# Optimization experiments

Hardware: AMD Instinct MI355X
Metric: run time of the kernel (lower is better)

Reference implementation:

```python
import jax, jax.numpy as jnp
import numpy as np

B, N, M, DK, DV, H = 4, 2048, 2048, 1024, 1024, 16
DKP = ((DK + H - 1) // H) * H  # 1024
DVP = ((DV + H - 1) // H) * H  # 1024


def setup_inputs() -> dict:
    key = jax.random.key(0)
    ks = jax.random.split(key, 12)
    s = 0.02
    return {
        "queries": jax.random.normal(ks[0], (B, N, DK), jnp.float32),
        "keys": jax.random.normal(ks[1], (B, M, DK), jnp.float32),
        "values": jax.random.normal(ks[2], (B, M, DV), jnp.float32),
        "presence": jnp.ones((B, M), jnp.float32),
        "n_heads": H,
        "wq": jax.random.normal(ks[3], (DK, DKP), jnp.float32) * s,
        "bq": jnp.zeros((DKP,), jnp.float32),
        "wk": jax.random.normal(ks[4], (DK, DKP), jnp.float32) * s,
        "bk": jnp.zeros((DKP,), jnp.float32),
        "wv": jax.random.normal(ks[5], (DV, DVP), jnp.float32) * s,
        "bv": jnp.zeros((DVP,), jnp.float32),
        "wo": jax.random.normal(ks[6], (DVP, DV), jnp.float32) * s,
        "bo": jnp.zeros((DV,), jnp.float32),
    }


def reference(queries, keys, values, presence, n_heads, wq, bq, wk, bk, wv, bv, wo, bo):
    b, n, _ = queries.shape
    m = keys.shape[1]
    h = n_heads
    # projections
    q = (queries @ wq + bq).reshape(b, n, h, -1)  # [B,N,H,dh]
    k = (keys @ wk + bk).reshape(b, m, h, -1)     # [B,M,H,dh]
    v = (values @ wv + bv).reshape(b, m, h, -1)   # [B,M,H,dv]
    dh = q.shape[-1]
    # scores: per-head scale is sqrt(per-head key dim), as in qkv_attention
    logits = jnp.einsum("bnhd,bmhd->bhnm", q, k)
    logits = logits - (1.0 - presence)[:, None, None, :] * 1e32
    attn = jax.nn.softmax(logits / jnp.sqrt(jnp.asarray(dh, logits.dtype)), axis=-1)
    o = jnp.einsum("bhnm,bmhd->bnhd", attn, v).reshape(b, n, -1)  # [B,N,DVP]
    return o @ wo + bo
```

## Files before the change

kernel.cpp:

```cpp
#include <hip/hip_runtime.h>


#define DI __device__ __forceinline__

typedef float f32x4 __attribute__((ext_vector_type(4)));
typedef __bf16 bf16x8 __attribute__((ext_vector_type(8)));
typedef __bf16 bf16x2 __attribute__((ext_vector_type(2)));
typedef unsigned short ushort8v __attribute__((ext_vector_type(8)));
typedef unsigned int uint4v __attribute__((ext_vector_type(4)));

typedef const __attribute__((address_space(1))) void gvoid_t;
typedef __attribute__((address_space(3))) void lvoid_t;

DI unsigned short f2b(float f) { return __builtin_bit_cast(unsigned short, (__bf16)f); }

DI unsigned pack2(float a, float b) {
  bf16x2 v;
  v[0] = (__bf16)a;
  v[1] = (__bf16)b;
  return __builtin_bit_cast(unsigned, v);
}

DI void swap32(unsigned& x, unsigned& y) {
  asm volatile("v_permlane32_swap_b32 %0, %1" : "+v"(x), "+v"(y));
}
DI void swap16(unsigned& x, unsigned& y) {
  asm volatile("v_permlane16_swap_b32 %0, %1" : "+v"(x), "+v"(y));
}

DI void gload16(const void* g, void* l) {
  __builtin_amdgcn_global_load_lds((gvoid_t*)g, (lvoid_t*)l, 16, 0, 0);
}

__global__ __launch_bounds__(256) void cvt_kernel(const float* __restrict__ in,
                                                  unsigned short* __restrict__ out, int n4) {
  int i = blockIdx.x * 256 + threadIdx.x;
  if (i < n4) {
    float4 v = ((const float4*)in)[i];
    ushort4 o;
    o.x = f2b(v.x); o.y = f2b(v.y); o.z = f2b(v.z); o.w = f2b(v.w);
    ((ushort4*)out)[i] = o;
  }
}

__global__ __launch_bounds__(256) void mask_kernel(const float* __restrict__ pres,
                                                   float* __restrict__ pm, int n) {
  int i = blockIdx.x * 256 + threadIdx.x;
  if (i < n) pm[i] = (pres[i] - 1.0f) * 1.8033688011112042e31f;
}

__global__ __launch_bounds__(256) void wtrans_kernel(const float* __restrict__ in,
                                                     unsigned short* __restrict__ out) {
  __shared__ float t[32][33];
  const int n0 = blockIdx.x * 32, k0 = blockIdx.y * 32;
  const int tx = threadIdx.x, ty = threadIdx.y;
#pragma unroll
  for (int i = 0; i < 4; ++i)
    t[ty + i * 8][tx] = in[(size_t)(k0 + ty + i * 8) * 1024 + n0 + tx];
  __syncthreads();
#pragma unroll
  for (int i = 0; i < 4; ++i)
    out[(size_t)(n0 + ty + i * 8) * 1024 + k0 + tx] = f2b(t[tx][ty + i * 8]);
}

__global__ __launch_bounds__(256) void vtrans_kernel(const unsigned short* __restrict__ vb,
                                                     unsigned short* __restrict__ vTg) {
  __shared__ unsigned short t[64][66];
  const int m0 = blockIdx.x * 64;
  const int h = blockIdx.y, b = blockIdx.z;
  const int tid = (int)threadIdx.x;
#pragma unroll
  for (int i = 0; i < 2; ++i) {
    int idx = i * 256 + tid;
    int row = idx >> 3;
    int d0 = (idx & 7) * 8;
    ushort8v v = *(const ushort8v*)(vb + ((size_t)(b * 2048 + m0 + row) * 16 + h) * 64 + d0);
#pragma unroll
    for (int j = 0; j < 8; ++j) t[row][d0 + j] = v[j];
  }
  __syncthreads();
#pragma unroll
  for (int i = 0; i < 2; ++i) {
    int idx = i * 256 + tid;
    int d = idx >> 3;
    int mo = (idx & 7) * 8;
    ushort8v o;
#pragma unroll
    for (int j = 0; j < 8; ++j) o[j] = t[mo + j][d];
    *(ushort8v*)(vTg + (((size_t)(b * 16 + h) * 64 + d) * 2048 + m0 + mo)) = o;
  }
}

template <typename CT>
__global__ __launch_bounds__(256, 2) void gemm_bt_kernel(const unsigned short* __restrict__ A,
                                                         const unsigned short* __restrict__ Bt,
                                                         const float* __restrict__ bias,
                                                         CT* __restrict__ C, int Ng, int Kg) {
  __shared__ unsigned short ldsA[128 * 64];
  __shared__ unsigned short ldsB[128 * 64];

  const int nbx = Ng >> 7;
  const int nwg = gridDim.x;
  const int cpx = nwg >> 3;
  const int wg0 = (int)blockIdx.x;
  const int wg = (wg0 & 7) * cpx + (wg0 >> 3);
  const int by = wg / nbx, bx = wg % nbx;

  const int tid = (int)threadIdx.x;
  const int w = tid >> 6, lane = tid & 63;
  const int lq = lane >> 4, lr = lane & 15;
  const int wr = w >> 1, wc = w & 1;

  const size_t rowA = (size_t)by * 128;
  const int colB = bx * 128;

  f32x4 acc[4][4];
#pragma unroll
  for (int m = 0; m < 4; ++m)
#pragma unroll
    for (int n = 0; n < 4; ++n) acc[m][n] = f32x4{0.f, 0.f, 0.f, 0.f};

  for (int k0 = 0; k0 < Kg; k0 += 64) {
#pragma unroll
    for (int i = 0; i < 4; ++i) {
      const int c = w * 4 + i;
      const int off = c * 1024 + lane * 16;
      const int row = off >> 7;
      const int kbs = (off & 127) ^ ((row & 7) << 4);
      gload16(A + ((rowA + row) * (size_t)Kg + k0 + (kbs >> 1)), &ldsA[c * 512]);
      gload16(Bt + ((size_t)(colB + row) * Kg + k0 + (kbs >> 1)), &ldsB[c * 512]);
    }
    __syncthreads();
#pragma unroll
    for (int kk = 0; kk < 2; ++kk) {
      const int kbyte = kk * 64 + lq * 16;
      bf16x8 af[4], bfv[4];
#pragma unroll
      for (int m = 0; m < 4; ++m) {
        const int row = wr * 64 + m * 16 + lr;
        af[m] = *(const bf16x8*)((const char*)ldsA + row * 128 + (kbyte ^ ((row & 7) << 4)));
      }
#pragma unroll
      for (int n = 0; n < 4; ++n) {
        const int row = wc * 64 + n * 16 + lr;
        bfv[n] = *(const bf16x8*)((const char*)ldsB + row * 128 + (kbyte ^ ((row & 7) << 4)));
      }
#pragma unroll
      for (int m = 0; m < 4; ++m)
#pragma unroll
        for (int n = 0; n < 4; ++n)
          acc[m][n] = __builtin_amdgcn_mfma_f32_16x16x32_bf16(af[m], bfv[n], acc[m][n], 0, 0, 0);
    }
    __syncthreads();
  }

#pragma unroll
  for (int n = 0; n < 4; ++n) {
    const int col = colB + wc * 64 + n * 16 + lr;
    const float bvl = bias[col];
#pragma unroll
    for (int m = 0; m < 4; ++m) {
      const size_t r0 = rowA + wr * 64 + m * 16 + lq * 4;
#pragma unroll
      for (int r = 0; r < 4; ++r) {
        const float v = acc[m][n][r] + bvl;
        if constexpr (sizeof(CT) == 2)
          C[(r0 + r) * Ng + col] = f2b(v);
        else
          C[(r0 + r) * Ng + col] = v;
      }
    }
  }
}

DI void softmax_pk(f32x4 s[4], float& mrun, float& lrun, f32x4 acc[4], unsigned* pk) {
  float rm = fmaxf(fmaxf(s[0][0], s[0][1]), fmaxf(s[0][2], s[0][3]));
#pragma unroll
  for (int kf = 1; kf < 4; ++kf)
    rm = fmaxf(rm, fmaxf(fmaxf(s[kf][0], s[kf][1]), fmaxf(s[kf][2], s[kf][3])));
  rm = fmaxf(rm, __shfl_xor(rm, 16, 64));
  rm = fmaxf(rm, __shfl_xor(rm, 32, 64));
  if (__any(rm > mrun + 8.0f)) {
    const float mn = fmaxf(mrun, rm);
    const float al = __builtin_amdgcn_exp2f(mrun - mn);
    lrun *= al;
#pragma unroll
    for (int df = 0; df < 4; ++df) acc[df] *= al;
    mrun = mn;
  }
  float rs = 0.f;
#pragma unroll
  for (int kf = 0; kf < 4; ++kf) {
#pragma unroll
    for (int r = 0; r < 4; ++r) {
      const float p = __builtin_amdgcn_exp2f(s[kf][r] - mrun);
      s[kf][r] = p;
      rs += p;
    }
    pk[kf * 2] = pack2(s[kf][0], s[kf][1]);
    pk[kf * 2 + 1] = pack2(s[kf][2], s[kf][3]);
  }
  rs += __shfl_xor(rs, 16, 64);
  rs += __shfl_xor(rs, 32, 64);
  lrun += rs;
}

DI bf16x8 pv_frag(const unsigned* pk, int kc) {
  unsigned x0 = pk[4 * kc + 0], y0 = pk[4 * kc + 2];
  swap32(x0, y0);
  swap16(x0, y0);
  unsigned x1 = pk[4 * kc + 1], y1 = pk[4 * kc + 3];
  swap32(x1, y1);
  swap16(x1, y1);
  uint4v wds;
  wds[0] = x0; wds[1] = x1; wds[2] = y0; wds[3] = y1;
  return __builtin_bit_cast(bf16x8, wds);
}

__global__ __launch_bounds__(256, 4) void attn_kernel(const unsigned short* __restrict__ Q,
                                                      const unsigned short* __restrict__ K,
                                                      const unsigned short* __restrict__ Vt,
                                                      const float* __restrict__ pm,
                                                      unsigned short* __restrict__ O) {
  __shared__ unsigned short kT[64 * 64];
  __shared__ unsigned short vT[64 * 64];

  const int q0 = blockIdx.x * 128;
  const int h = blockIdx.y, b = blockIdx.z;
  const int tid = (int)threadIdx.x;
  const int w = tid >> 6, lane = tid & 63;
  const int lq = lane >> 4, lr = lane & 15;

  const unsigned short* qp = Q + ((size_t)(b * 2048 + q0 + w * 32 + lr) * 1024 + h * 64);
  const bf16x8 qfA0 = *(const bf16x8*)(qp + lq * 8);
  const bf16x8 qfA1 = *(const bf16x8*)(qp + 32 + lq * 8);
  const bf16x8 qfB0 = *(const bf16x8*)(qp + 16384 + lq * 8);
  const bf16x8 qfB1 = *(const bf16x8*)(qp + 16384 + 32 + lq * 8);

  const int s7 = (lr & 7) << 4;
  const int rd0 = lr * 128 + ((lq * 16) ^ s7);
  const int rd1 = lr * 128 + ((64 + lq * 16) ^ s7);

  const int rowS0 = w * 16 + (lane >> 3), rowS1 = rowS0 + 8;
  const int colS0 = ((lane & 7) * 16) ^ ((rowS0 & 7) << 4);
  const int colS1 = ((lane & 7) * 16) ^ ((rowS1 & 7) << 4);
  const unsigned short* Kb = K + (size_t)(b * 2048) * 1024 + h * 64;
  const unsigned short* Vb = Vt + (size_t)((b * 16 + h) * 64) * 2048;
  const float* pmB = pm + b * 2048;

  f32x4 accA[4], accB[4];
#pragma unroll
  for (int df = 0; df < 4; ++df) {
    accA[df] = f32x4{0.f, 0.f, 0.f, 0.f};
    accB[df] = f32x4{0.f, 0.f, 0.f, 0.f};
  }
  float mA = -3.0e38f, lA = 0.f, mB = -3.0e38f, lB = 0.f;

  for (int m0 = 0; m0 < 2048; m0 += 64) {
    gload16(Kb + (size_t)(m0 + rowS0) * 1024 + (colS0 >> 1), &kT[(w * 2) * 512]);
    gload16(Vb + (size_t)rowS0 * 2048 + m0 + (colS0 >> 1), &vT[(w * 2) * 512]);
    gload16(Kb + (size_t)(m0 + rowS1) * 1024 + (colS1 >> 1), &kT[(w * 2 + 1) * 512]);
    gload16(Vb + (size_t)rowS1 * 2048 + m0 + (colS1 >> 1), &vT[(w * 2 + 1) * 512]);
    __syncthreads();

    f32x4 sA[4], sB[4];
#pragma unroll
    for (int kf = 0; kf < 4; ++kf) {
      sA[kf] = f32x4{0.f, 0.f, 0.f, 0.f};
      sB[kf] = f32x4{0.f, 0.f, 0.f, 0.f};
    }
#pragma unroll
    for (int kk = 0; kk < 2; ++kk) {
      const int rdk = kk ? rd1 : rd0;
      const bf16x8 qa = kk ? qfA1 : qfA0;
      const bf16x8 qb = kk ? qfB1 : qfB0;
#pragma unroll
      for (int kf = 0; kf < 4; ++kf) {
        const bf16x8 kfr = *(const bf16x8*)((const char*)kT + rdk + kf * 2048);
        sA[kf] = __builtin_amdgcn_mfma_f32_16x16x32_bf16(kfr, qa, sA[kf], 0, 0, 0);
        sB[kf] = __builtin_amdgcn_mfma_f32_16x16x32_bf16(kfr, qb, sB[kf], 0, 0, 0);
      }
    }

    const float SC = 0.18033688011112042f;
#pragma unroll
    for (int kf = 0; kf < 4; ++kf) {
      const f32x4 pv = *(const f32x4*)(pmB + m0 + kf * 16 + lq * 4);
#pragma unroll
      for (int r = 0; r < 4; ++r) {
        sA[kf][r] = sA[kf][r] * SC + pv[r];
        sB[kf][r] = sB[kf][r] * SC + pv[r];
      }
    }

    unsigned pkA[8], pkB[8];
    softmax_pk(sA, mA, lA, accA, pkA);
    softmax_pk(sB, mB, lB, accB, pkB);

#pragma unroll
    for (int kc = 0; kc < 2; ++kc) {
      const int rdk = kc ? rd1 : rd0;
      const bf16x8 pa = pv_frag(pkA, kc);
      const bf16x8 pb = pv_frag(pkB, kc);
#pragma unroll
      for (int df = 0; df < 4; ++df) {
        const bf16x8 vf = *(const bf16x8*)((const char*)vT + rdk + df * 2048);
        accA[df] = __builtin_amdgcn_mfma_f32_16x16x32_bf16(vf, pa, accA[df], 0, 0, 0);
        accB[df] = __builtin_amdgcn_mfma_f32_16x16x32_bf16(vf, pb, accB[df], 0, 0, 0);
      }
    }
    __syncthreads();
  }

  const float rlA = __builtin_amdgcn_rcpf(lA);
  const float rlB = __builtin_amdgcn_rcpf(lB);
  unsigned short* Op = O + ((size_t)(b * 2048 + q0 + w * 32 + lr) * 1024 + h * 64);
#pragma unroll
  for (int df = 0; df < 4; ++df) {
    ushort4 oa, ob;
    oa.x = f2b(accA[df][0] * rlA); oa.y = f2b(accA[df][1] * rlA);
    oa.z = f2b(accA[df][2] * rlA); oa.w = f2b(accA[df][3] * rlA);
    ob.x = f2b(accB[df][0] * rlB); ob.y = f2b(accB[df][1] * rlB);
    ob.z = f2b(accB[df][2] * rlB); ob.w = f2b(accB[df][3] * rlB);
    *(ushort4*)(Op + df * 16 + lq * 4) = oa;
    *(ushort4*)(Op + 16384 + df * 16 + lq * 4) = ob;
  }
}

extern "C" void kernel_launch(void* const* d_in, const int* in_sizes, int n_in,
                              void* d_out, int out_size, void* d_ws, size_t ws_size,
                              hipStream_t stream) {
  const float* queries = (const float*)d_in[0];
  const float* keys = (const float*)d_in[1];
  const float* values = (const float*)d_in[2];
  const float* presence = (const float*)d_in[3];
  const float* wq = (const float*)d_in[5];
  const float* bq = (const float*)d_in[6];
  const float* wk = (const float*)d_in[7];
  const float* bk = (const float*)d_in[8];
  const float* wv = (const float*)d_in[9];
  const float* bv = (const float*)d_in[10];
  const float* wo = (const float*)d_in[11];
  const float* bo = (const float*)d_in[12];
  float* out = (float*)d_out;

  char* ws = (char*)d_ws;
  unsigned short* inb = (unsigned short*)(ws + (size_t)0);
  unsigned short* qb = (unsigned short*)(ws + (size_t)16777216);
  unsigned short* kb = (unsigned short*)(ws + (size_t)33554432);
  unsigned short* vb = (unsigned short*)(ws + (size_t)50331648);
  unsigned short* vTg = (unsigned short*)(ws + (size_t)67108864);
  unsigned short* wqT = (unsigned short*)(ws + (size_t)83886080);
  unsigned short* wkT = wqT + 1048576;
  unsigned short* wvT = wkT + 1048576;
  unsigned short* woT = wvT + 1048576;
  float* pmb = (float*)(ws + (size_t)92274688);

  const dim3 wtg(32, 32), wtb(32, 8);
  const dim3 vtg(32, 16, 4);
  const dim3 atg(16, 16, 4);
  const int cvtBlocks = 8192;

  mask_kernel<<<32, 256, 0, stream>>>(presence, pmb, 8192);

  cvt_kernel<<<cvtBlocks, 256, 0, stream>>>(queries, inb, 2097152);
  wtrans_kernel<<<wtg, wtb, 0, stream>>>(wq, wqT);
  gemm_bt_kernel<unsigned short><<<512, 256, 0, stream>>>(inb, wqT, bq, qb, 1024, 1024);

  cvt_kernel<<<cvtBlocks, 256, 0, stream>>>(keys, inb, 2097152);
  wtrans_kernel<<<wtg, wtb, 0, stream>>>(wk, wkT);
  gemm_bt_kernel<unsigned short><<<512, 256, 0, stream>>>(inb, wkT, bk, kb, 1024, 1024);

  cvt_kernel<<<cvtBlocks, 256, 0, stream>>>(values, inb, 2097152);
  wtrans_kernel<<<wtg, wtb, 0, stream>>>(wv, wvT);
  gemm_bt_kernel<unsigned short><<<512, 256, 0, stream>>>(inb, wvT, bv, vb, 1024, 1024);

  vtrans_kernel<<<vtg, 256, 0, stream>>>(vb, vTg);

  attn_kernel<<<atg, 256, 0, stream>>>(qb, kb, vTg, pmb, inb);

  wtrans_kernel<<<wtg, wtb, 0, stream>>>(wo, woT);
  gemm_bt_kernel<float><<<512, 256, 0, stream>>>(inb, woT, bo, out, 1024, 1024);
}
```

Baseline: 386.0 us.

## Batch QKV conversion, weight transposes and projections; fuse V transpose into GEMM epilogue

Replaces three separate convert, transpose and GEMM launches with single batched launches over a z dimension, so each projection grid covers 1536 workgroups instead of 512. The V projection epilogue now writes directly into the head-transposed layout, which removes the separate vtrans kernel and its round trip through global memory. Launch bounds are raised to 3 waves per SIMD to increase occupancy. The cost is a larger workspace and strided 8-byte stores in the V epilogue.

```diff
diff --git a/kernel.cpp b/kernel.cpp
--- a/kernel.cpp
+++ b/kernel.cpp
@@ -32,15 +32,20 @@
   __builtin_amdgcn_global_load_lds((gvoid_t*)g, (lvoid_t*)l, 16, 0, 0);
 }
 
-__global__ __launch_bounds__(256) void cvt_kernel(const float* __restrict__ in,
-                                                  unsigned short* __restrict__ out, int n4) {
+__global__ __launch_bounds__(256) void cvt3_kernel(const float* __restrict__ q,
+                                                   const float* __restrict__ k,
+                                                   const float* __restrict__ v,
+                                                   unsigned short* __restrict__ qo,
+                                                   unsigned short* __restrict__ ko,
+                                                   unsigned short* __restrict__ vo) {
+  const int z = blockIdx.y;
+  const float* in = z == 0 ? q : z == 1 ? k : v;
+  unsigned short* out = z == 0 ? qo : z == 1 ? ko : vo;
   int i = blockIdx.x * 256 + threadIdx.x;
-  if (i < n4) {
-    float4 v = ((const float4*)in)[i];
-    ushort4 o;
-    o.x = f2b(v.x); o.y = f2b(v.y); o.z = f2b(v.z); o.w = f2b(v.w);
-    ((ushort4*)out)[i] = o;
-  }
+  float4 vv = ((const float4*)in)[i];
+  ushort4 o;
+  o.x = f2b(vv.x); o.y = f2b(vv.y); o.z = f2b(vv.z); o.w = f2b(vv.w);
+  ((ushort4*)out)[i] = o;
 }
 
 __global__ __launch_bounds__(256) void mask_kernel(const float* __restrict__ pres,
@@ -49,9 +54,18 @@
   if (i < n) pm[i] = (pres[i] - 1.0f) * 1.8033688011112042e31f;
 }
 
-__global__ __launch_bounds__(256) void wtrans_kernel(const float* __restrict__ in,
-                                                     unsigned short* __restrict__ out) {
+__global__ __launch_bounds__(256) void wtrans4_kernel(const float* __restrict__ w0,
+                                                      const float* __restrict__ w1,
+                                                      const float* __restrict__ w2,
+                                                      const float* __restrict__ w3,
+                                                      unsigned short* __restrict__ o0,
+                                                      unsigned short* __restrict__ o1,
+                                                      unsigned short* __restrict__ o2,
+                                                      unsigned short* __restrict__ o3) {
   __shared__ float t[32][33];
+  const int z = blockIdx.z;
+  const float* in = z == 0 ? w0 : z == 1 ? w1 : z == 2 ? w2 : w3;
+  unsigned short* out = z == 0 ? o0 : z == 1 ? o1 : z == 2 ? o2 : o3;
   const int n0 = blockIdx.x * 32, k0 = blockIdx.y * 32;
   const int tx = threadIdx.x, ty = threadIdx.y;
 #pragma unroll
@@ -63,45 +77,24 @@
     out[(size_t)(n0 + ty + i * 8) * 1024 + k0 + tx] = f2b(t[tx][ty + i * 8]);
 }
 
-__global__ __launch_bounds__(256) void vtrans_kernel(const unsigned short* __restrict__ vb,
-                                                     unsigned short* __restrict__ vTg) {
-  __shared__ unsigned short t[64][66];
-  const int m0 = blockIdx.x * 64;
-  const int h = blockIdx.y, b = blockIdx.z;
-  const int tid = (int)threadIdx.x;
-#pragma unroll
-  for (int i = 0; i < 2; ++i) {
-    int idx = i * 256 + tid;
-    int row = idx >> 3;
-    int d0 = (idx & 7) * 8;
-    ushort8v v = *(const ushort8v*)(vb + ((size_t)(b * 2048 + m0 + row) * 16 + h) * 64 + d0);
-#pragma unroll
-    for (int j = 0; j < 8; ++j) t[row][d0 + j] = v[j];
-  }
-  __syncthreads();
-#pragma unroll
-  for (int i = 0; i < 2; ++i) {
-    int idx = i * 256 + tid;
-    int d = idx >> 3;
-    int mo = (idx & 7) * 8;
-    ushort8v o;
-#pragma unroll
-    for (int j = 0; j < 8; ++j) o[j] = t[mo + j][d];
-    *(ushort8v*)(vTg + (((size_t)(b * 16 + h) * 64 + d) * 2048 + m0 + mo)) = o;
-  }
-}
-
-template <typename CT>
-__global__ __launch_bounds__(256, 2) void gemm_bt_kernel(const unsigned short* __restrict__ A,
-                                                         const unsigned short* __restrict__ Bt,
-                                                         const float* __restrict__ bias,
-                                                         CT* __restrict__ C, int Ng, int Kg) {
+
+__global__ __launch_bounds__(256, 3) void gemm_qkv_kernel(
+    const unsigned short* __restrict__ qin, const unsigned short* __restrict__ kin,
+    const unsigned short* __restrict__ vin, const unsigned short* __restrict__ wqT,
+    const unsigned short* __restrict__ wkT, const unsigned short* __restrict__ wvT,
+    const float* __restrict__ bq, const float* __restrict__ bk,
+    const float* __restrict__ bv, unsigned short* __restrict__ qb,
+    unsigned short* __restrict__ kb, unsigned short* __restrict__ vTg) {
   __shared__ unsigned short ldsA[128 * 64];
   __shared__ unsigned short ldsB[128 * 64];
 
-  const int nbx = Ng >> 7;
-  const int nwg = gridDim.x;
-  const int cpx = nwg >> 3;
+  const int z = blockIdx.z;
+  const unsigned short* A = z == 0 ? qin : z == 1 ? kin : vin;
+  const unsigned short* Bt = z == 0 ? wqT : z == 1 ? wkT : wvT;
+  const float* bias = z == 0 ? bq : z == 1 ? bk : bv;
+
+  const int nbx = 8;
+  const int cpx = 64;
   const int wg0 = (int)blockIdx.x;
   const int wg = (wg0 & 7) * cpx + (wg0 >> 3);
   const int by = wg / nbx, bx = wg % nbx;
@@ -120,15 +113,15 @@
 #pragma unroll
     for (int n = 0; n < 4; ++n) acc[m][n] = f32x4{0.f, 0.f, 0.f, 0.f};
 
-  for (int k0 = 0; k0 < Kg; k0 += 64) {
+  for (int k0 = 0; k0 < 1024; k0 += 64) {
 #pragma unroll
     for (int i = 0; i < 4; ++i) {
       const int c = w * 4 + i;
       const int off = c * 1024 + lane * 16;
       const int row = off >> 7;
       const int kbs = (off & 127) ^ ((row & 7) << 4);
-      gload16(A + ((rowA + row) * (size_t)Kg + k0 + (kbs >> 1)), &ldsA[c * 512]);
-      gload16(Bt + ((size_t)(colB + row) * Kg + k0 + (kbs >> 1)), &ldsB[c * 512]);
+      gload16(A + ((rowA + row) * 1024 + k0 + (kbs >> 1)), &ldsA[c * 512]);
+      gload16(Bt + ((size_t)(colB + row) * 1024 + k0 + (kbs >> 1)), &ldsB[c * 512]);
     }
     __syncthreads();
 #pragma unroll
@@ -154,6 +147,101 @@
     __syncthreads();
   }
 
+  if (z < 2) {
+    unsigned short* C = z == 0 ? qb : kb;
+#pragma unroll
+    for (int n = 0; n < 4; ++n) {
+      const int col = colB + wc * 64 + n * 16 + lr;
+      const float bvl = bias[col];
+#pragma unroll
+      for (int m = 0; m < 4; ++m) {
+        const size_t r0 = rowA + wr * 64 + m * 16 + lq * 4;
+#pragma unroll
+        for (int r = 0; r < 4; ++r) C[(r0 + r) * 1024 + col] = f2b(acc[m][n][r] + bvl);
+      }
+    }
+  } else {
+#pragma unroll
+    for (int n = 0; n < 4; ++n) {
+      const int col = colB + wc * 64 + n * 16 + lr;
+      const float bvl = bias[col];
+#pragma unroll
+      for (int m = 0; m < 4; ++m) {
+        const size_t row0 = rowA + wr * 64 + m * 16 + lq * 4;
+        const int bb = (int)(row0 >> 11);
+        const int ml = (int)(row0 & 2047);
+        ushort4 o;
+        o.x = f2b(acc[m][n][0] + bvl);
+        o.y = f2b(acc[m][n][1] + bvl);
+        o.z = f2b(acc[m][n][2] + bvl);
+        o.w = f2b(acc[m][n][3] + bvl);
+        *(ushort4*)(vTg + (((size_t)(bb * 1024 + col)) << 11) + ml) = o;
+      }
+    }
+  }
+}
+
+__global__ __launch_bounds__(256, 3) void gemm_bt_kernel(const unsigned short* __restrict__ A,
+                                                         const unsigned short* __restrict__ Bt,
+                                                         const float* __restrict__ bias,
+                                                         float* __restrict__ C) {
+  __shared__ unsigned short ldsA[128 * 64];
+  __shared__ unsigned short ldsB[128 * 64];
+
+  const int nbx = 8;
+  const int cpx = 64;
+  const int wg0 = (int)blockIdx.x;
+  const int wg = (wg0 & 7) * cpx + (wg0 >> 3);
+  const int by = wg / nbx, bx = wg % nbx;
+
+  const int tid = (int)threadIdx.x;
+  const int w = tid >> 6, lane = tid & 63;
+  const int lq = lane >> 4, lr = lane & 15;
+  const int wr = w >> 1, wc = w & 1;
+
+  const size_t rowA = (size_t)by * 128;
+  const int colB = bx * 128;
+
+  f32x4 acc[4][4];
+#pragma unroll
+  for (int m = 0; m < 4; ++m)
+#pragma unroll
+    for (int n = 0; n < 4; ++n) acc[m][n] = f32x4{0.f, 0.f, 0.f, 0.f};
+
+  for (int k0 = 0; k0 < 1024; k0 += 64) {
+#pragma unroll
+    for (int i = 0; i < 4; ++i) {
+      const int c = w * 4 + i;
+      const int off = c * 1024 + lane * 16;
+      const int row = off >> 7;
+      const int kbs = (off & 127) ^ ((row & 7) << 4);
+      gload16(A + ((rowA + row) * 1024 + k0 + (kbs >> 1)), &ldsA[c * 512]);
+      gload16(Bt + ((size_t)(colB + row) * 1024 + k0 + (kbs >> 1)), &ldsB[c * 512]);
+    }
+    __syncthreads();
+#pragma unroll
+    for (int kk = 0; kk < 2; ++kk) {
+      const int kbyte = kk * 64 + lq * 16;
+      bf16x8 af[4], bfv[4];
+#pragma unroll
+      for (int m = 0; m < 4; ++m) {
+        const int row = wr * 64 + m * 16 + lr;
+        af[m] = *(const bf16x8*)((const char*)ldsA + row * 128 + (kbyte ^ ((row & 7) << 4)));
+      }
+#pragma unroll
+      for (int n = 0; n < 4; ++n) {
+        const int row = wc * 64 + n * 16 + lr;
+        bfv[n] = *(const bf16x8*)((const char*)ldsB + row * 128 + (kbyte ^ ((row & 7) << 4)));
+      }
+#pragma unroll
+      for (int m = 0; m < 4; ++m)
+#pragma unroll
+        for (int n = 0; n < 4; ++n)
+          acc[m][n] = __builtin_amdgcn_mfma_f32_16x16x32_bf16(af[m], bfv[n], acc[m][n], 0, 0, 0);
+    }
+    __syncthreads();
+  }
+
 #pragma unroll
   for (int n = 0; n < 4; ++n) {
     const int col = colB + wc * 64 + n * 16 + lr;
@@ -162,13 +250,7 @@
     for (int m = 0; m < 4; ++m) {
       const size_t r0 = rowA + wr * 64 + m * 16 + lq * 4;
 #pragma unroll
-      for (int r = 0; r < 4; ++r) {
-        const float v = acc[m][n][r] + bvl;
-        if constexpr (sizeof(CT) == 2)
-          C[(r0 + r) * Ng + col] = f2b(v);
-        else
-          C[(r0 + r) * Ng + col] = v;
-      }
+      for (int r = 0; r < 4; ++r) C[(r0 + r) * 1024 + col] = acc[m][n][r] + bvl;
     }
   }
 }
@@ -273,12 +355,12 @@
     for (int kk = 0; kk < 2; ++kk) {
       const int rdk = kk ? rd1 : rd0;
       const bf16x8 qa = kk ? qfA1 : qfA0;
-      const bf16x8 qb = kk ? qfB1 : qfB0;
+      const bf16x8 qb_ = kk ? qfB1 : qfB0;
 #pragma unroll
       for (int kf = 0; kf < 4; ++kf) {
         const bf16x8 kfr = *(const bf16x8*)((const char*)kT + rdk + kf * 2048);
         sA[kf] = __builtin_amdgcn_mfma_f32_16x16x32_bf16(kfr, qa, sA[kf], 0, 0, 0);
-        sB[kf] = __builtin_amdgcn_mfma_f32_16x16x32_bf16(kfr, qb, sB[kf], 0, 0, 0);
+        sB[kf] = __builtin_amdgcn_mfma_f32_16x16x32_bf16(kfr, qb_, sB[kf], 0, 0, 0);
       }
     }
 
@@ -345,40 +427,25 @@
   float* out = (float*)d_out;
 
   char* ws = (char*)d_ws;
-  unsigned short* inb = (unsigned short*)(ws + (size_t)0);
-  unsigned short* qb = (unsigned short*)(ws + (size_t)16777216);
-  unsigned short* kb = (unsigned short*)(ws + (size_t)33554432);
-  unsigned short* vb = (unsigned short*)(ws + (size_t)50331648);
-  unsigned short* vTg = (unsigned short*)(ws + (size_t)67108864);
-  unsigned short* wqT = (unsigned short*)(ws + (size_t)83886080);
-  unsigned short* wkT = wqT + 1048576;
-  unsigned short* wvT = wkT + 1048576;
-  unsigned short* woT = wvT + 1048576;
-  float* pmb = (float*)(ws + (size_t)92274688);
-
-  const dim3 wtg(32, 32), wtb(32, 8);
-  const dim3 vtg(32, 16, 4);
-  const dim3 atg(16, 16, 4);
-  const int cvtBlocks = 8192;
+  const size_t MB = 1048576;
+  unsigned short* qin = (unsigned short*)(ws + 0 * MB);
+  unsigned short* kin = (unsigned short*)(ws + 16 * MB);
+  unsigned short* vin = (unsigned short*)(ws + 32 * MB);
+  unsigned short* qb = (unsigned short*)(ws + 48 * MB);
+  unsigned short* kb = (unsigned short*)(ws + 64 * MB);
+  unsigned short* vTg = (unsigned short*)(ws + 80 * MB);
+  unsigned short* wqT = (unsigned short*)(ws + 96 * MB);
+  unsigned short* wkT = (unsigned short*)(ws + 98 * MB);
+  unsigned short* wvT = (unsigned short*)(ws + 100 * MB);
+  unsigned short* woT = (unsigned short*)(ws + 102 * MB);
+  float* pmb = (float*)(ws + 104 * MB);
 
   mask_kernel<<<32, 256, 0, stream>>>(presence, pmb, 8192);
-
-  cvt_kernel<<<cvtBlocks, 256, 0, stream>>>(queries, inb, 2097152);
-  wtrans_kernel<<<wtg, wtb, 0, stream>>>(wq, wqT);
-  gemm_bt_kernel<unsigned short><<<512, 256, 0, stream>>>(inb, wqT, bq, qb, 1024, 1024);
-
-  cvt_kernel<<<cvtBlocks, 256, 0, stream>>>(keys, inb, 2097152);
-  wtrans_kernel<<<wtg, wtb, 0, stream>>>(wk, wkT);
-  gemm_bt_kernel<unsigned short><<<512, 256, 0, stream>>>(inb, wkT, bk, kb, 1024, 1024);
-
-  cvt_kernel<<<cvtBlocks, 256, 0, stream>>>(values, inb, 2097152);
-  wtrans_kernel<<<wtg, wtb, 0, stream>>>(wv, wvT);
-  gemm_bt_kernel<unsigned short><<<512, 256, 0, stream>>>(inb, wvT, bv, vb, 1024, 1024);
-
-  vtrans_kernel<<<vtg, 256, 0, stream>>>(vb, vTg);
-
-  attn_kernel<<<atg, 256, 0, stream>>>(qb, kb, vTg, pmb, inb);
-
-  wtrans_kernel<<<wtg, wtb, 0, stream>>>(wo, woT);
-  gemm_bt_kernel<float><<<512, 256, 0, stream>>>(inb, woT, bo, out, 1024, 1024);
-}
+  cvt3_kernel<<<dim3(8192, 3), 256, 0, stream>>>(queries, keys, values, qin, kin, vin);
+  wtrans4_kernel<<<dim3(32, 32, 4), dim3(32, 8), 0, stream>>>(wq, wk, wv, wo, wqT, wkT, wvT,
+                                                              woT);
+  gemm_qkv_kernel<<<dim3(512, 1, 3), 256, 0, stream>>>(qin, kin, vin, wqT, wkT, wvT, bq, bk,
+                                                       bv, qb, kb, vTg);
+  attn_kernel<<<dim3(16, 16, 4), 256, 0, stream>>>(qb, kb, vTg, pmb, qin);
+  gemm_bt_kernel<<<512, 256, 0, stream>>>(qin, woT, bo, out);
+}
```

After: 374.7 us. -2.9%, faster.
